# Kernel optimization log

Hardware: AMD Instinct MI355X
Metric: run time of the kernel (lower is better)

## Reference

```python
import jax, jax.numpy as jnp
from jax import lax
import numpy as np

V = 50000          # num_word; embedding table has V+1 rows
D = 512            # embedding_dim / d_model
H = 8              # nhead
FF = 2048          # dim_feedforward (hidden_dim)
L = 32             # num_label (incl START/STOP)
START, STOP = L - 2, L - 1
S = 2048           # sentence length
NEG = -10000.0


def setup_inputs() -> dict:
    k = jax.random.split(jax.random.key(0), 10)
    def rn(key, shape, s=0.02):
        return jax.random.normal(key, shape, jnp.float32) * s
    transitions = jax.random.normal(k[8], (L, L), jnp.float32)
    transitions = transitions.at[START, :].set(NEG).at[:, STOP].set(NEG)
    return {
        "sentence": jax.random.randint(k[0], (S,), 0, V + 1),
        "embed": rn(k[1], (V + 1, D), 1.0),
        "Wqkv": rn(k[2], (3 * D, D)), "bqkv": jnp.zeros((3 * D,), jnp.float32),
        "Wo": rn(k[3], (D, D)), "bo": jnp.zeros((D,), jnp.float32),
        "ln1_g": jnp.ones((D,), jnp.float32), "ln1_b": jnp.zeros((D,), jnp.float32),
        "W1": rn(k[4], (FF, D)), "b1": jnp.zeros((FF,), jnp.float32),
        "W2": rn(k[5], (D, FF)), "b2": jnp.zeros((D,), jnp.float32),
        "ln2_g": jnp.ones((D,), jnp.float32), "ln2_b": jnp.zeros((D,), jnp.float32),
        "Wt": rn(k[6], (L, D)), "bt": jnp.zeros((L,), jnp.float32),
        "transitions": transitions,
    }


def _ln(x, g, b):
    m = jnp.mean(x, -1, keepdims=True)
    v = jnp.var(x, -1, keepdims=True)
    return (x - m) * lax.rsqrt(v + 1e-5) * g + b


def _transformer_feats(sentence, embed, Wqkv, bqkv, Wo, bo, ln1_g, ln1_b,
                       W1, b1, W2, b2, ln2_g, ln2_b, Wt, bt):
    x = embed[sentence]                                   # [S, D]
    qkv = x @ Wqkv.T + bqkv                               # [S, 3D]
    q, k, v = jnp.split(qkv, 3, axis=-1)
    to_heads = lambda t: t.reshape(S, H, D // H).transpose(1, 0, 2)  # [H, S, dh]
    q, k, v = to_heads(q), to_heads(k), to_heads(v)
    att = jax.nn.softmax(jnp.einsum('hsd,htd->hst', q, k) / np.float32(np.sqrt(D // H)), axis=-1)
    o = jnp.einsum('hst,htd->hsd', att, v).transpose(1, 0, 2).reshape(S, D)
    # post-norm TransformerEncoderLayer (eval mode: dropout off), relu FFN
    x = _ln(x + o @ Wo.T + bo, ln1_g, ln1_b)
    ff = jax.nn.relu(x @ W1.T + b1) @ W2.T + b2
    x = _ln(x + ff, ln2_g, ln2_b)
    return x @ Wt.T + bt                                  # [S, L] emission scores


def _viterbi(feats, transitions):
    init = jnp.full((L,), NEG, jnp.float32).at[START].set(0.0)
    def step(prev, emit):
        scores = prev[None, :] + transitions              # [next_tag, prev_tag]
        bp = jnp.argmax(scores, axis=1)                   # best prev tag per next tag
        return jnp.max(scores, axis=1) + emit, bp
    last, bps = lax.scan(step, init, feats)               # bps: [S, L]
    terminal = last + transitions[STOP]
    best = jnp.argmax(terminal)
    def back(tag, bp):
        return bp[tag], tag
    _, path = lax.scan(back, best, bps, reverse=True)     # path[t] = best tag at step t
    return terminal[best], path


def reference(sentence, embed, Wqkv, bqkv, Wo, bo, ln1_g, ln1_b,
              W1, b1, W2, b2, ln2_g, ln2_b, Wt, bt, transitions):
    feats = _transformer_feats(sentence, embed, Wqkv, bqkv, Wo, bo, ln1_g, ln1_b,
                               W1, b1, W2, b2, ln2_g, ln2_b, Wt, bt)
    score, path = _viterbi(feats, transitions)
    return score, path
```

## Files before the change

### kernel.cpp

```cpp
#include <hip/hip_runtime.h>
#include <cstddef>

#define S_LEN 2048
#define D_MODEL 512
#define NHEAD 8
#define DH 64
#define FF_DIM 2048
#define L_TAGS 32
#define START_TAG 30
#define STOP_TAG 31
#define NEGV (-10000.0f)
#define QSCALE 0.18033688f

typedef unsigned int uint2v __attribute__((ext_vector_type(2)));
typedef __attribute__((ext_vector_type(8))) short short8v;
typedef __attribute__((ext_vector_type(4))) float f32x4;

union U8 { uint4 u; short8v s; };

__device__ __forceinline__ unsigned short f2bf(float f) {
  unsigned u = __float_as_uint(f);
  u += 0x7fff + ((u >> 16) & 1);
  return (unsigned short)(u >> 16);
}
__device__ __forceinline__ unsigned cvtpk(float lo, float hi) {
  unsigned r;
  asm("v_cvt_pk_bf16_f32 %0, %1, %2" : "=v"(r) : "v"(lo), "v"(hi));
  return r;
}

__global__ __launch_bounds__(256) void k_f2h4(const float* __restrict__ s0, short* __restrict__ d0,
                                              const float* __restrict__ s1, short* __restrict__ d1,
                                              const float* __restrict__ s2, short* __restrict__ d2,
                                              const float* __restrict__ s3, short* __restrict__ d3) {
  const int b = blockIdx.x;
  const float* src; short* dst; int i;
  if (b < 384)       { src = s0; dst = d0; i = b * 256 + threadIdx.x; }
  else if (b < 512)  { src = s1; dst = d1; i = (b - 384) * 256 + threadIdx.x; }
  else if (b < 1024) { src = s2; dst = d2; i = (b - 512) * 256 + threadIdx.x; }
  else               { src = s3; dst = d3; i = (b - 1024) * 256 + threadIdx.x; }
  f32x4 a = *(const f32x4*)(src + (size_t)i * 8);
  f32x4 c = *(const f32x4*)(src + (size_t)i * 8 + 4);
  U8 t;
  t.u.x = cvtpk(a[0], a[1]); t.u.y = cvtpk(a[2], a[3]);
  t.u.z = cvtpk(c[0], c[1]); t.u.w = cvtpk(c[2], c[3]);
  *(short8v*)(dst + (size_t)i * 8) = t.s;
}

__global__ __launch_bounds__(256, 2) void k_gemm_qkv(const int* __restrict__ sent,
                                                     const float* __restrict__ embed,
                                                     const short* __restrict__ B,
                                                     const float* __restrict__ bias,
                                                     short* __restrict__ C,
                                                     int N, int K) {
  __shared__ __align__(16) short As[2][128 * 64];
  __shared__ __align__(16) short Bs[2][128 * 64];
  const int tid = threadIdx.x;
  const int nwg = gridDim.x * gridDim.y;
  int lin = blockIdx.x + gridDim.x * blockIdx.y;
  int wk = (lin & 7) * (nwg >> 3) + (lin >> 3);
  const int bxs = wk % gridDim.x, bys = wk / gridDim.x;
  const int bm = bys * 128, bn = bxs * 128;
  const int w = tid >> 6, lane = tid & 63;
  const int wr = w >> 1, wc = w & 1;
  const int fr = lane & 15, kg = lane >> 4;
  const int srow = tid >> 1, sc0 = (tid & 1) * 4;
  const int swz = srow & 7;
  const float* gA = embed + (size_t)sent[bm + srow] * K + sc0 * 8;
  const short* gB = B + (size_t)(bn + srow) * K + sc0 * 8;
  f32x4 ra[8];
  short8v rb[4];
  f32x4 acc[4][4] = {};

  auto loadg = [&](int k0) {
#pragma unroll
    for (int c = 0; c < 4; ++c) {
      ra[2 * c] = *(const f32x4*)(gA + k0 + c * 8);
      ra[2 * c + 1] = *(const f32x4*)(gA + k0 + c * 8 + 4);
      rb[c] = *(const short8v*)(gB + k0 + c * 8);
    }
  };
  auto storeb = [&](int b) {
    short* dA = &As[b][srow * 64];
    short* dB = &Bs[b][srow * 64];
#pragma unroll
    for (int c = 0; c < 4; ++c) {
      U8 ta;
      ta.u.x = cvtpk(ra[2 * c][0], ra[2 * c][1]);
      ta.u.y = cvtpk(ra[2 * c][2], ra[2 * c][3]);
      ta.u.z = cvtpk(ra[2 * c + 1][0], ra[2 * c + 1][1]);
      ta.u.w = cvtpk(ra[2 * c + 1][2], ra[2 * c + 1][3]);
      *(short8v*)(dA + (((sc0 + c) ^ swz) << 3)) = ta.s;
      *(short8v*)(dB + (((sc0 + c) ^ swz) << 3)) = rb[c];
    }
  };

  loadg(0);
  storeb(0);
  __syncthreads();
  int cur = 0;
  const int fswz = fr & 7;
  for (int k0 = 0; k0 < K; k0 += 64) {
    const bool more = (k0 + 64) < K;
    if (more) loadg(k0 + 64);
    const short* rA = &As[cur][(wr * 64 + fr) * 64];
    const short* rB = &Bs[cur][(wc * 64 + fr) * 64];
#pragma unroll
    for (int ks = 0; ks < 2; ++ks) {
      const int co = ((ks * 4 + kg) ^ fswz) << 3;
      short8v af[4], bf[4];
#pragma unroll
      for (int rt = 0; rt < 4; ++rt) af[rt] = *(const short8v*)(rA + rt * 16 * 64 + co);
#pragma unroll
      for (int ct = 0; ct < 4; ++ct) bf[ct] = *(const short8v*)(rB + ct * 16 * 64 + co);
#pragma unroll
      for (int rt = 0; rt < 4; ++rt)
#pragma unroll
        for (int ct = 0; ct < 4; ++ct)
          acc[rt][ct] = __builtin_amdgcn_mfma_f32_16x16x32_bf16(af[rt], bf[ct], acc[rt][ct], 0, 0, 0);
    }
    if (more) storeb(cur ^ 1);
    __syncthreads();
    cur ^= 1;
  }
#pragma unroll
  for (int rt = 0; rt < 4; ++rt) {
#pragma unroll
    for (int ct = 0; ct < 4; ++ct) {
      f32x4 v = acc[rt][ct];
      const int row0 = bm + wr * 64 + rt * 16 + kg * 4;
      const int col = bn + wc * 64 + ct * 16 + fr;
      const float bs = bias[col];
#pragma unroll
      for (int j = 0; j < 4; ++j)
        C[(size_t)(row0 + j) * N + col] = (short)f2bf(v[j] + bs);
    }
  }
}

template <int RT, bool RELU, bool OBF>
__global__ __launch_bounds__(256, 2) void k_gemm_bf(const short* __restrict__ A,
                                                    const short* __restrict__ B,
                                                    const float* __restrict__ bias,
                                                    void* __restrict__ Cp,
                                                    int M, int N, int K) {
  constexpr int BM = RT * 32;
  constexpr int CH = (BM * 8) / 256;
  __shared__ __align__(16) short As[2][BM * 64];
  __shared__ __align__(16) short Bs[2][BM * 64];
  const int tid = threadIdx.x;
  const int nwg = gridDim.x * gridDim.y;
  int lin = blockIdx.x + gridDim.x * blockIdx.y;
  int wk = (lin & 7) * (nwg >> 3) + (lin >> 3);
  const int bxs = wk % gridDim.x, bys = wk / gridDim.x;
  const int bm = bys * BM, bn = bxs * BM;
  const int w = tid >> 6, lane = tid & 63;
  const int wr = w >> 1, wc = w & 1;
  const int fr = lane & 15, kg = lane >> 4;
  const int srow = (RT == 4) ? (tid >> 1) : (tid >> 2);
  const int sc0 = (RT == 4) ? ((tid & 1) * 4) : ((tid & 3) * 2);
  const int swz = srow & 7;
  const short* gA = A + (size_t)(bm + srow) * K + sc0 * 8;
  const short* gB = B + (size_t)(bn + srow) * K + sc0 * 8;
  short8v ra[CH], rb[CH];
  f32x4 acc[RT][RT] = {};

  auto loadg = [&](int k0) {
#pragma unroll
    for (int c = 0; c < CH; ++c) {
      ra[c] = *(const short8v*)(gA + k0 + c * 8);
      rb[c] = *(const short8v*)(gB + k0 + c * 8);
    }
  };
  auto storeb = [&](int b) {
    short* dA = &As[b][srow * 64];
    short* dB = &Bs[b][srow * 64];
#pragma unroll
    for (int c = 0; c < CH; ++c) {
      *(short8v*)(dA + (((sc0 + c) ^ swz) << 3)) = ra[c];
      *(short8v*)(dB + (((sc0 + c) ^ swz) << 3)) = rb[c];
    }
  };

  loadg(0);
  storeb(0);
  __syncthreads();
  int cur = 0;
  const int fswz = fr & 7;
  for (int k0 = 0; k0 < K; k0 += 64) {
    const bool more = (k0 + 64) < K;
    if (more) loadg(k0 + 64);
    const short* rA = &As[cur][(wr * (RT * 16) + fr) * 64];
    const short* rB = &Bs[cur][(wc * (RT * 16) + fr) * 64];
#pragma unroll
    for (int ks = 0; ks < 2; ++ks) {
      const int co = ((ks * 4 + kg) ^ fswz) << 3;
      short8v af[RT], bf[RT];
#pragma unroll
      for (int rt = 0; rt < RT; ++rt) af[rt] = *(const short8v*)(rA + rt * 16 * 64 + co);
#pragma unroll
      for (int ct = 0; ct < RT; ++ct) bf[ct] = *(const short8v*)(rB + ct * 16 * 64 + co);
#pragma unroll
      for (int rt = 0; rt < RT; ++rt)
#pragma unroll
        for (int ct = 0; ct < RT; ++ct)
          acc[rt][ct] = __builtin_amdgcn_mfma_f32_16x16x32_bf16(af[rt], bf[ct], acc[rt][ct], 0, 0, 0);
    }
    if (more) storeb(cur ^ 1);
    __syncthreads();
    cur ^= 1;
  }
#pragma unroll
  for (int rt = 0; rt < RT; ++rt) {
#pragma unroll
    for (int ct = 0; ct < RT; ++ct) {
      f32x4 v = acc[rt][ct];
      const int row0 = bm + wr * (RT * 16) + rt * 16 + kg * 4;
      const int col = bn + wc * (RT * 16) + ct * 16 + fr;
      const float bs = bias[col];
#pragma unroll
      for (int j = 0; j < 4; ++j) {
        float o = v[j] + bs;
        if (RELU) o = fmaxf(o, 0.f);
        if (OBF)
          ((short*)Cp)[(size_t)(row0 + j) * N + col] = (short)f2bf(o);
        else
          ((float*)Cp)[(size_t)(row0 + j) * N + col] = o;
      }
    }
  }
}

__global__ __launch_bounds__(256) void k_attn(const short* __restrict__ qkv,
                                              short* __restrict__ ob) {
  __shared__ __align__(16) short Ks[2][64 * 64];
  __shared__ __align__(16) short Vt[2][64 * 72];
  __shared__ __align__(16) short Pl[4][16 * 72];
  const int tid = threadIdx.x;
  const int b = blockIdx.x;
  const int h = b & 7;
  const int bq = (b >> 3) * 64;
  const int wq = tid >> 6, lane = tid & 63;
  const int fr = lane & 15, kg = lane >> 4;
  auto scale8 = [](short8v q) -> short8v {
    unsigned wv[4];
#pragma unroll
    for (int i = 0; i < 4; ++i) {
      float lo = __uint_as_float(((unsigned)(unsigned short)q[2 * i]) << 16) * QSCALE;
      float hi = __uint_as_float(((unsigned)(unsigned short)q[2 * i + 1]) << 16) * QSCALE;
      wv[i] = cvtpk(lo, hi);
    }
    U8 t;
    t.u.x = wv[0]; t.u.y = wv[1]; t.u.z = wv[2]; t.u.w = wv[3];
    return t.s;
  };
  short8v qf[2];
  {
    const short* qsrc = qkv + (size_t)(bq + wq * 16 + fr) * 1536 + h * DH;
    qf[0] = scale8(*(const short8v*)(qsrc + kg * 8));
    qf[1] = scale8(*(const short8v*)(qsrc + 32 + kg * 8));
  }
  float m[4], ls[4];
  f32x4 oac[4] = {};
#pragma unroll
  for (int j = 0; j < 4; ++j) { m[j] = -1e30f; ls[j] = 0.f; }

  const int srow = tid >> 2, sc0 = (tid & 3) * 2;
  const int kpair = tid & 31, dgrp = tid >> 5;
  short8v kr0, kr1, va, vb;
  auto loadt = [&](int kt) {
    const short* kbase = qkv + (size_t)(kt * 64 + srow) * 1536 + 512 + h * DH;
    kr0 = *(const short8v*)(kbase + sc0 * 8);
    kr1 = *(const short8v*)(kbase + sc0 * 8 + 8);
    const short* vbase = qkv + (size_t)(kt * 64 + 2 * kpair) * 1536 + 1024 + h * DH + dgrp * 8;
    va = *(const short8v*)(vbase);
    vb = *(const short8v*)(vbase + 1536);
  };
  auto storet = [&](int cu) {
    short* dk = &Ks[cu][srow * 64];
    *(short8v*)(dk + ((sc0 ^ (srow & 7)) << 3)) = kr0;
    *(short8v*)(dk + (((sc0 + 1) ^ (srow & 7)) << 3)) = kr1;
#pragma unroll
    for (int i = 0; i < 8; ++i) {
      unsigned u = ((unsigned)(unsigned short)va[i]) |
                   (((unsigned)(unsigned short)vb[i]) << 16);
      *(unsigned*)&Vt[cu][(dgrp * 8 + i) * 72 + 2 * kpair] = u;
    }
  };

  loadt(0);
  int cur = 0;
  for (int kt = 0; kt < 32; ++kt) {
    storet(cur);
    __syncthreads();
    if (kt < 31) loadt(kt + 1);
    f32x4 sac[4] = {};
#pragma unroll
    for (int ks = 0; ks < 2; ++ks) {
#pragma unroll
      for (int ct = 0; ct < 4; ++ct) {
        const int row = ct * 16 + fr;
        short8v bfr = *(const short8v*)&Ks[cur][row * 64 + (((ks * 4 + kg) ^ (row & 7)) << 3)];
        sac[ct] = __builtin_amdgcn_mfma_f32_16x16x32_bf16(qf[ks], bfr, sac[ct], 0, 0, 0);
      }
    }
    float pv[4][4];
#pragma unroll
    for (int j = 0; j < 4; ++j) {
      float v = fmaxf(fmaxf(sac[0][j], sac[1][j]), fmaxf(sac[2][j], sac[3][j]));
#pragma unroll
      for (int off = 1; off < 16; off <<= 1) v = fmaxf(v, __shfl_xor(v, off, 64));
      float mn = fmaxf(m[j], v);
      float f = __builtin_amdgcn_exp2f(m[j] - mn);
      m[j] = mn;
      float rs = 0.f;
#pragma unroll
      for (int ct = 0; ct < 4; ++ct) {
        pv[ct][j] = __builtin_amdgcn_exp2f(sac[ct][j] - mn);
        rs += pv[ct][j];
      }
      ls[j] = ls[j] * f + rs;
#pragma unroll
      for (int ct = 0; ct < 4; ++ct) oac[ct][j] *= f;
    }
#pragma unroll
    for (int ct = 0; ct < 4; ++ct)
#pragma unroll
      for (int j = 0; j < 4; ++j)
        Pl[wq][(kg * 4 + j) * 72 + ct * 16 + fr] = (short)f2bf(pv[ct][j]);
#pragma unroll
    for (int ks = 0; ks < 2; ++ks) {
      short8v paf = *(const short8v*)&Pl[wq][fr * 72 + ks * 32 + kg * 8];
#pragma unroll
      for (int ct = 0; ct < 4; ++ct) {
        short8v vf = *(const short8v*)&Vt[cur][(ct * 16 + fr) * 72 + ks * 32 + kg * 8];
        oac[ct] = __builtin_amdgcn_mfma_f32_16x16x32_bf16(paf, vf, oac[ct], 0, 0, 0);
      }
    }
    cur ^= 1;
  }
#pragma unroll
  for (int j = 0; j < 4; ++j) {
#pragma unroll
    for (int off = 1; off < 16; off <<= 1) ls[j] += __shfl_xor(ls[j], off, 64);
    float inv = 1.f / ls[j];
    const int q = bq + wq * 16 + kg * 4 + j;
#pragma unroll
    for (int ct = 0; ct < 4; ++ct)
      ob[(size_t)q * D_MODEL + h * DH + ct * 16 + fr] = (short)f2bf(oac[ct][j] * inv);
  }
}

__global__ __launch_bounds__(128) void k_ln(const float* __restrict__ a,
                                            const int* __restrict__ sent,
                                            const float* __restrict__ embed,
                                            const float* __restrict__ r,
                                            const float* __restrict__ g,
                                            const float* __restrict__ b,
                                            float* __restrict__ out,
                                            short* __restrict__ outh) {
  __shared__ float red[2];
  const int row = blockIdx.x, tid = threadIdx.x;
  const size_t off = (size_t)row * D_MODEL + tid * 4;
  float4 av;
  if (sent)
    av = *(const float4*)(embed + (size_t)sent[row] * D_MODEL + tid * 4);
  else
    av = *(const float4*)(a + off);
  float4 rv = *(const float4*)(r + off);
  float v0 = av.x + rv.x, v1 = av.y + rv.y, v2 = av.z + rv.z, v3 = av.w + rv.w;
  float s = v0 + v1 + v2 + v3;
#pragma unroll
  for (int d = 1; d < 64; d <<= 1) s += __shfl_xor(s, d, 64);
  if ((tid & 63) == 0) red[tid >> 6] = s;
  __syncthreads();
  float mean = (red[0] + red[1]) * (1.f / 512.f);
  __syncthreads();
  float d0 = v0 - mean, d1 = v1 - mean, d2 = v2 - mean, d3 = v3 - mean;
  float sq = d0 * d0 + d1 * d1 + d2 * d2 + d3 * d3;
#pragma unroll
  for (int d = 1; d < 64; d <<= 1) sq += __shfl_xor(sq, d, 64);
  if ((tid & 63) == 0) red[tid >> 6] = sq;
  __syncthreads();
  float inv = rsqrtf((red[0] + red[1]) * (1.f / 512.f) + 1e-5f);
  float4 gv = *(const float4*)(g + tid * 4);
  float4 bv = *(const float4*)(b + tid * 4);
  float4 o;
  o.x = d0 * inv * gv.x + bv.x;
  o.y = d1 * inv * gv.y + bv.y;
  o.z = d2 * inv * gv.z + bv.z;
  o.w = d3 * inv * gv.w + bv.w;
  *(float4*)(out + off) = o;
  if (outh) {
    uint2v t;
    t[0] = cvtpk(o.x, o.y);
    t[1] = cvtpk(o.z, o.w);
    *(uint2v*)(outh + off) = t;
  }
}

__global__ __launch_bounds__(128) void k_lnfeats(const float* __restrict__ a,
                                                 const float* __restrict__ r,
                                                 const float* __restrict__ g,
                                                 const float* __restrict__ b,
                                                 const float* __restrict__ Wt,
                                                 const float* __restrict__ bt,
                                                 float* __restrict__ feats) {
  __shared__ float red[2];
  __shared__ float part[2][32];
  const int row = blockIdx.x, tid = threadIdx.x;
  const size_t off = (size_t)row * D_MODEL + tid * 4;
  float4 av = *(const float4*)(a + off);
  float4 rv = *(const float4*)(r + off);
  float v0 = av.x + rv.x, v1 = av.y + rv.y, v2 = av.z + rv.z, v3 = av.w + rv.w;
  float s = v0 + v1 + v2 + v3;
#pragma unroll
  for (int d = 1; d < 64; d <<= 1) s += __shfl_xor(s, d, 64);
  if ((tid & 63) == 0) red[tid >> 6] = s;
  __syncthreads();
  float mean = (red[0] + red[1]) * (1.f / 512.f);
  __syncthreads();
  float d0 = v0 - mean, d1 = v1 - mean, d2 = v2 - mean, d3 = v3 - mean;
  float sq = d0 * d0 + d1 * d1 + d2 * d2 + d3 * d3;
#pragma unroll
  for (int d = 1; d < 64; d <<= 1) sq += __shfl_xor(sq, d, 64);
  if ((tid & 63) == 0) red[tid >> 6] = sq;
  __syncthreads();
  float inv = rsqrtf((red[0] + red[1]) * (1.f / 512.f) + 1e-5f);
  float4 gv = *(const float4*)(g + tid * 4);
  float4 bv = *(const float4*)(b + tid * 4);
  float4 o;
  o.x = d0 * inv * gv.x + bv.x;
  o.y = d1 * inv * gv.y + bv.y;
  o.z = d2 * inv * gv.z + bv.z;
  o.w = d3 * inv * gv.w + bv.w;
  const int lane = tid & 63, wv = tid >> 6;
#pragma unroll
  for (int l = 0; l < 32; ++l) {
    float4 wr4 = *(const float4*)(Wt + (size_t)l * D_MODEL + tid * 4);
    float p = o.x * wr4.x + o.y * wr4.y + o.z * wr4.z + o.w * wr4.w;
#pragma unroll
    for (int d = 1; d < 64; d <<= 1) p += __shfl_xor(p, d, 64);
    if (lane == 0) part[wv][l] = p;
  }
  __syncthreads();
  if (tid < 32) feats[(size_t)row * L_TAGS + tid] = part[0][tid] + part[1][tid] + bt[tid];
}

__global__ __launch_bounds__(64) void k_scan1(const float* __restrict__ feats,
                                              const float* __restrict__ T,
                                              float* __restrict__ P) {
  __shared__ float S[2][32];
  const int c = blockIdx.x >> 4;
  const int l = threadIdx.x;
  const int n = l & 31, pl = l >> 5;
  const int p = (blockIdx.x & 15) * 2 + pl;
  float Trow[32];
#pragma unroll
  for (int q = 0; q < 32; ++q) Trow[q] = T[n * 32 + q];
  const int tbase = c * 32;
  float er[4];
#pragma unroll
  for (int i = 0; i < 4; ++i) er[i] = feats[(tbase + i) * 32 + n];
  float a = T[n * 32 + p] + er[0];
  S[pl][n] = a;
  const float* fp = feats + (size_t)(tbase + 4) * 32 + n;
  er[0] = fp[0]; fp += 32;
  for (int u = 1; u < 32; ++u) {
    float e = er[u & 3];
    float enew = fp[0]; fp += 32;
    const float4* Sv = (const float4*)&S[pl][0];
    float g[32];
#pragma unroll
    for (int j4 = 0; j4 < 8; ++j4) {
      float4 sv = Sv[j4];
      g[j4 * 4 + 0] = sv.x + Trow[j4 * 4 + 0];
      g[j4 * 4 + 1] = sv.y + Trow[j4 * 4 + 1];
      g[j4 * 4 + 2] = sv.z + Trow[j4 * 4 + 2];
      g[j4 * 4 + 3] = sv.w + Trow[j4 * 4 + 3];
    }
#pragma unroll
    for (int st = 1; st < 32; st <<= 1)
#pragma unroll
      for (int j = 0; j < 32; j += 2 * st) g[j] = fmaxf(g[j], g[j + st]);
    a = g[0] + e;
    S[pl][n] = a;
    er[u & 3] = enew;
  }
  P[(size_t)c * 1024 + n * 32 + p] = a;
}

__global__ __launch_bounds__(64) void k_scan2(const float* __restrict__ P,
                                              const float* __restrict__ T,
                                              float* __restrict__ alphas,
                                              float* __restrict__ out,
                                              int* __restrict__ bestp) {
  __shared__ float Sa[32];
  const int l = threadIdx.x, n = l & 31, half = l >> 5;
  float a = (n == START_TAG) ? 0.f : NEGV;
  const float* pbase = P + n * 32 + half * 16;
  float4 pr[4];
#pragma unroll
  for (int j = 0; j < 4; ++j) pr[j] = *(const float4*)(pbase + j * 4);
  for (int c = 0; c < 64; ++c) {
    float4 nx[4];
#pragma unroll
    for (int j = 0; j < 4; ++j)
      nx[j] = *(const float4*)(pbase + (size_t)(c + 1) * 1024 + j * 4);
    alphas[(size_t)(c * 32) * 32 + n] = a;
    Sa[n] = a;
    const float4* Sv = (const float4*)&Sa[half * 16];
    float g[16];
#pragma unroll
    for (int j = 0; j < 4; ++j) {
      float4 sv = Sv[j];
      g[j * 4 + 0] = pr[j].x + sv.x;
      g[j * 4 + 1] = pr[j].y + sv.y;
      g[j * 4 + 2] = pr[j].z + sv.z;
      g[j * 4 + 3] = pr[j].w + sv.w;
    }
#pragma unroll
    for (int st = 1; st < 16; st <<= 1)
#pragma unroll
      for (int j = 0; j < 16; j += 2 * st) g[j] = fmaxf(g[j], g[j + st]);
    uint2v r = __builtin_amdgcn_permlane32_swap(__float_as_uint(g[0]),
                                                __float_as_uint(g[0]), false, false);
    a = fmaxf(__uint_as_float(r[0]), __uint_as_float(r[1]));
#pragma unroll
    for (int j = 0; j < 4; ++j) pr[j] = nx[j];
  }
  float term = a + T[STOP_TAG * 32 + n];
  float bv = term;
  int bi = n;
#pragma unroll
  for (int d = 1; d < 32; d <<= 1) {
    float ov = __shfl_xor(bv, d, 64);
    int oi = __shfl_xor(bi, d, 64);
    if (ov > bv || (ov == bv && oi < bi)) { bv = ov; bi = oi; }
  }
  if (l == 0) { out[0] = bv; *bestp = bi; }
}

__global__ __launch_bounds__(64) void k_scan3(const float* __restrict__ feats,
                                              const float* __restrict__ T,
                                              const float* __restrict__ alphas,
                                              unsigned char* __restrict__ cand,
                                              unsigned char* __restrict__ amap) {
  __shared__ float Sa[32];
  __shared__ unsigned char bpl[32][32];
  __shared__ unsigned cnd[256];
  const int c = blockIdx.x, l = threadIdx.x, n = l & 31, half = l >> 5;
  float Tr[16];
#pragma unroll
  for (int j = 0; j < 16; ++j) Tr[j] = T[n * 32 + half * 16 + j];
  const int tbase = c * 32;
  float a = alphas[(size_t)tbase * 32 + n];
  float er[4];
#pragma unroll
  for (int i = 0; i < 4; ++i) er[i] = feats[(tbase + i) * 32 + n];
  const float* fp = feats + (size_t)(tbase + 4) * 32 + n;
  Sa[n] = a;
  for (int u = 0; u < 32; ++u) {
    float e = er[u & 3];
    float enew = fp[0]; fp += 32;
    const float4* Sv = (const float4*)&Sa[half * 16];
    float4 s0 = Sv[0], s1 = Sv[1], s2 = Sv[2], s3 = Sv[3];
    float v[16] = {s0.x + Tr[0],  s0.y + Tr[1],  s0.z + Tr[2],  s0.w + Tr[3],
                   s1.x + Tr[4],  s1.y + Tr[5],  s1.z + Tr[6],  s1.w + Tr[7],
                   s2.x + Tr[8],  s2.y + Tr[9],  s2.z + Tr[10], s2.w + Tr[11],
                   s3.x + Tr[12], s3.y + Tr[13], s3.z + Tr[14], s3.w + Tr[15]};
    int id[16];
#pragma unroll
    for (int j = 0; j < 16; ++j) id[j] = half * 16 + j;
#pragma unroll
    for (int st = 1; st < 16; st <<= 1)
#pragma unroll
      for (int j = 0; j < 16; j += 2 * st)
        if (v[j + st] > v[j]) { v[j] = v[j + st]; id[j] = id[j + st]; }
    uint2v rv = __builtin_amdgcn_permlane32_swap(__float_as_uint(v[0]),
                                                 __float_as_uint(v[0]), false, false);
    uint2v ri = __builtin_amdgcn_permlane32_swap((unsigned)id[0], (unsigned)id[0],
                                                 false, false);
    float v0 = __uint_as_float(rv[0]), v1 = __uint_as_float(rv[1]);
    int i0 = (int)ri[0], i1 = (int)ri[1];
    float wvv = (v1 > v0) ? v1 : v0;
    int wi = (v1 > v0) ? i1 : i0;
    bpl[u][n] = (unsigned char)wi;
    a = wvv + e;
    Sa[n] = a;
    er[u & 3] = enew;
  }
  unsigned char* cnb = (unsigned char*)cnd;
  int tg = n;
  cnb[n * 32 + 31] = (unsigned char)n;
  for (int j = 31; j >= 1; --j) {
    tg = bpl[j][tg];
    cnb[n * 32 + (j - 1)] = (unsigned char)tg;
  }
  if (half == 0) amap[c * 32 + n] = bpl[0][tg];
#pragma unroll
  for (int i = 0; i < 4; ++i)
    ((unsigned*)(cand + (size_t)c * 1024))[l * 4 + i] = cnd[l * 4 + i];
}

__global__ __launch_bounds__(256) void k_trace2(const unsigned char* __restrict__ amap,
                                                const unsigned char* __restrict__ cand,
                                                const int* __restrict__ bestp,
                                                float* __restrict__ outp) {
  __shared__ unsigned char Am[64][32];
  __shared__ unsigned char et[64];
  const int tid = threadIdx.x;
  ((unsigned*)&Am[0][0])[tid] = ((const unsigned*)amap)[tid];
  ((unsigned*)&Am[32][0])[tid] = ((const unsigned*)amap)[tid + 256];
  __syncthreads();
  for (int d = 1; d < 64; d <<= 1) {
    unsigned char tmpv[8];
#pragma unroll
    for (int i = 0; i < 8; ++i) {
      int id = tid + 256 * i;
      int cc = id >> 5, e = id & 31;
      tmpv[i] = (cc + d < 64) ? Am[cc][Am[cc + d][e]] : Am[cc][e];
    }
    __syncthreads();
#pragma unroll
    for (int i = 0; i < 8; ++i) {
      int id = tid + 256 * i;
      Am[id >> 5][id & 31] = tmpv[i];
    }
    __syncthreads();
  }
  const int best = *bestp;
  if (tid < 64) et[tid] = (tid == 63) ? (unsigned char)best : Am[tid + 1][best];
  __syncthreads();
#pragma unroll
  for (int i = 0; i < 8; ++i) {
    int t = tid + 256 * i;
    int cc = t >> 5, j = t & 31;
    outp[1 + t] = (float)cand[(size_t)cc * 1024 + (size_t)et[cc] * 32 + j];
  }
}

extern "C" void kernel_launch(void* const* d_in, const int* in_sizes, int n_in,
                              void* d_out, int out_size, void* d_ws, size_t ws_size,
                              hipStream_t stream) {
  (void)in_sizes; (void)n_in; (void)out_size; (void)ws_size;
  const int* sent = (const int*)d_in[0];
  const float* embed = (const float*)d_in[1];
  const float* Wqkv = (const float*)d_in[2];
  const float* bqkv = (const float*)d_in[3];
  const float* Wo = (const float*)d_in[4];
  const float* bo = (const float*)d_in[5];
  const float* g1 = (const float*)d_in[6];
  const float* b1n = (const float*)d_in[7];
  const float* W1 = (const float*)d_in[8];
  const float* b1f = (const float*)d_in[9];
  const float* W2 = (const float*)d_in[10];
  const float* b2f = (const float*)d_in[11];
  const float* g2 = (const float*)d_in[12];
  const float* b2n = (const float*)d_in[13];
  const float* Wt = (const float*)d_in[14];
  const float* bt = (const float*)d_in[15];
  const float* T = (const float*)d_in[16];
  float* out = (float*)d_out;

  float* ws = (float*)d_ws;
  const size_t M1 = 1u << 20;
  short* qkvh = (short*)ws;
  short* obh = (short*)(ws + 2 * M1);
  float* yb = ws + 3 * M1;
  float* x1 = ws + 4 * M1;
  short* x1h = (short*)(ws + 5 * M1);
  short* ffbh = (short*)(ws + 6 * M1);
  float* zb = ws + 8 * M1;
  short* wqkvh = (short*)(ws + 10 * M1);
  short* woh = wqkvh + 786432;
  short* w1h = woh + 262144;
  short* w2h = w1h + 1048576;
  float* feats = ws + 11 * M1;
  float* alphas = feats + 2048 * 32 + 64;
  float* P = alphas + 2049 * 32 + 64;
  int* bestp = (int*)(P + 65 * 1024 + 64);
  unsigned char* cand = (unsigned char*)(bestp + 64);
  unsigned char* amap = cand + 2048 * 32;

  k_f2h4<<<dim3(1536), dim3(256), 0, stream>>>(Wqkv, wqkvh, Wo, woh, W1, w1h, W2, w2h);
  k_gemm_qkv<<<dim3(12, 16), dim3(256), 0, stream>>>(sent, embed, wqkvh, bqkv, qkvh, 1536, 512);
  k_attn<<<dim3(256), dim3(256), 0, stream>>>(qkvh, obh);
  k_gemm_bf<2, false, false><<<dim3(8, 32), dim3(256), 0, stream>>>(obh, woh, bo, yb, 2048, 512, 512);
  k_ln<<<dim3(2048), dim3(128), 0, stream>>>(nullptr, sent, embed, yb, g1, b1n, x1, x1h);
  k_gemm_bf<4, true, true><<<dim3(16, 16), dim3(256), 0, stream>>>(x1h, w1h, b1f, ffbh, 2048, 2048, 512);
  k_gemm_bf<2, false, false><<<dim3(8, 32), dim3(256), 0, stream>>>(ffbh, w2h, b2f, zb, 2048, 512, 2048);
  k_lnfeats<<<dim3(2048), dim3(128), 0, stream>>>(x1, zb, g2, b2n, Wt, bt, feats);
  k_scan1<<<dim3(1024), dim3(64), 0, stream>>>(feats, T, P);
  k_scan2<<<dim3(1), dim3(64), 0, stream>>>(P, T, alphas, out, bestp);
  k_scan3<<<dim3(64), dim3(64), 0, stream>>>(feats, T, alphas, cand, amap);
  k_trace2<<<dim3(1), dim3(256), 0, stream>>>(amap, cand, bestp, out);
}
```

Before: 179.1 us.

## Halve attention query tile to 32 rows, add MFMA priority and lazy rescale

The attention kernel now runs 512 blocks of 128 threads, each covering 32 query rows instead of 64, so more blocks are available to fill the compute units. Each thread now loads four K chunks and two V pairs per tile. MFMA sections are wrapped in s_setprio so matrix work is favoured over other waves. The online softmax skips the rescale of the output accumulator when no row maximum increases across the wavefront. The cost is that every K/V tile is loaded twice as often overall, raising global and LDS traffic per unit of compute.

Result: slower. 206.4 us (+15.2%).

```diff
diff --git a/kernel.cpp b/kernel.cpp
--- a/kernel.cpp
+++ b/kernel.cpp
@@ -231,15 +231,15 @@
   }
 }
 
-__global__ __launch_bounds__(256) void k_attn(const short* __restrict__ qkv,
+__global__ __launch_bounds__(128) void k_attn(const short* __restrict__ qkv,
                                               short* __restrict__ ob) {
   __shared__ __align__(16) short Ks[2][64 * 64];
   __shared__ __align__(16) short Vt[2][64 * 72];
-  __shared__ __align__(16) short Pl[4][16 * 72];
+  __shared__ __align__(16) short Pl[2][16 * 72];
   const int tid = threadIdx.x;
   const int b = blockIdx.x;
   const int h = b & 7;
-  const int bq = (b >> 3) * 64;
+  const int bq = (b >> 3) * 32;
   const int wq = tid >> 6, lane = tid & 63;
   const int fr = lane & 15, kg = lane >> 4;
   auto scale8 = [](short8v q) -> short8v {
@@ -265,26 +265,32 @@
 #pragma unroll
   for (int j = 0; j < 4; ++j) { m[j] = -1e30f; ls[j] = 0.f; }
 
-  const int srow = tid >> 2, sc0 = (tid & 3) * 2;
+  const int srow = tid >> 1, sc0 = (tid & 1) * 4;
   const int kpair = tid & 31, dgrp = tid >> 5;
-  short8v kr0, kr1, va, vb;
+  short8v kr[4], va0, vb0, va1, vb1;
   auto loadt = [&](int kt) {
     const short* kbase = qkv + (size_t)(kt * 64 + srow) * 1536 + 512 + h * DH;
-    kr0 = *(const short8v*)(kbase + sc0 * 8);
-    kr1 = *(const short8v*)(kbase + sc0 * 8 + 8);
+#pragma unroll
+    for (int c = 0; c < 4; ++c) kr[c] = *(const short8v*)(kbase + (sc0 + c) * 8);
     const short* vbase = qkv + (size_t)(kt * 64 + 2 * kpair) * 1536 + 1024 + h * DH + dgrp * 8;
-    va = *(const short8v*)(vbase);
-    vb = *(const short8v*)(vbase + 1536);
+    va0 = *(const short8v*)(vbase);
+    vb0 = *(const short8v*)(vbase + 1536);
+    va1 = *(const short8v*)(vbase + 32);
+    vb1 = *(const short8v*)(vbase + 1536 + 32);
   };
   auto storet = [&](int cu) {
     short* dk = &Ks[cu][srow * 64];
-    *(short8v*)(dk + ((sc0 ^ (srow & 7)) << 3)) = kr0;
-    *(short8v*)(dk + (((sc0 + 1) ^ (srow & 7)) << 3)) = kr1;
+#pragma unroll
+    for (int c = 0; c < 4; ++c)
+      *(short8v*)(dk + (((sc0 + c) ^ (srow & 7)) << 3)) = kr[c];
 #pragma unroll
     for (int i = 0; i < 8; ++i) {
-      unsigned u = ((unsigned)(unsigned short)va[i]) |
-                   (((unsigned)(unsigned short)vb[i]) << 16);
-      *(unsigned*)&Vt[cu][(dgrp * 8 + i) * 72 + 2 * kpair] = u;
+      unsigned u0 = ((unsigned)(unsigned short)va0[i]) |
+                    (((unsigned)(unsigned short)vb0[i]) << 16);
+      unsigned u1 = ((unsigned)(unsigned short)va1[i]) |
+                    (((unsigned)(unsigned short)vb1[i]) << 16);
+      *(unsigned*)&Vt[cu][(dgrp * 8 + i) * 72 + 2 * kpair] = u0;
+      *(unsigned*)&Vt[cu][((dgrp + 4) * 8 + i) * 72 + 2 * kpair] = u1;
     }
   };
 
@@ -295,6 +301,7 @@
     __syncthreads();
     if (kt < 31) loadt(kt + 1);
     f32x4 sac[4] = {};
+    __builtin_amdgcn_s_setprio(1);
 #pragma unroll
     for (int ks = 0; ks < 2; ++ks) {
 #pragma unroll
@@ -304,30 +311,41 @@
         sac[ct] = __builtin_amdgcn_mfma_f32_16x16x32_bf16(qf[ks], bfr, sac[ct], 0, 0, 0);
       }
     }
+    __builtin_amdgcn_s_setprio(0);
     float pv[4][4];
 #pragma unroll
     for (int j = 0; j < 4; ++j) {
       float v = fmaxf(fmaxf(sac[0][j], sac[1][j]), fmaxf(sac[2][j], sac[3][j]));
 #pragma unroll
       for (int off = 1; off < 16; off <<= 1) v = fmaxf(v, __shfl_xor(v, off, 64));
-      float mn = fmaxf(m[j], v);
-      float f = __builtin_amdgcn_exp2f(m[j] - mn);
-      m[j] = mn;
       float rs = 0.f;
-#pragma unroll
-      for (int ct = 0; ct < 4; ++ct) {
-        pv[ct][j] = __builtin_amdgcn_exp2f(sac[ct][j] - mn);
-        rs += pv[ct][j];
+      if (__all(v <= m[j])) {
+#pragma unroll
+        for (int ct = 0; ct < 4; ++ct) {
+          pv[ct][j] = __builtin_amdgcn_exp2f(sac[ct][j] - m[j]);
+          rs += pv[ct][j];
+        }
+        ls[j] += rs;
+      } else {
+        float mn = fmaxf(m[j], v);
+        float f = __builtin_amdgcn_exp2f(m[j] - mn);
+        m[j] = mn;
+#pragma unroll
+        for (int ct = 0; ct < 4; ++ct) {
+          pv[ct][j] = __builtin_amdgcn_exp2f(sac[ct][j] - mn);
+          rs += pv[ct][j];
+        }
+        ls[j] = ls[j] * f + rs;
+#pragma unroll
+        for (int ct = 0; ct < 4; ++ct) oac[ct][j] *= f;
       }
-      ls[j] = ls[j] * f + rs;
-#pragma unroll
-      for (int ct = 0; ct < 4; ++ct) oac[ct][j] *= f;
     }
 #pragma unroll
     for (int ct = 0; ct < 4; ++ct)
 #pragma unroll
       for (int j = 0; j < 4; ++j)
         Pl[wq][(kg * 4 + j) * 72 + ct * 16 + fr] = (short)f2bf(pv[ct][j]);
+    __builtin_amdgcn_s_setprio(1);
 #pragma unroll
     for (int ks = 0; ks < 2; ++ks) {
       short8v paf = *(const short8v*)&Pl[wq][fr * 72 + ks * 32 + kg * 8];
@@ -337,6 +355,7 @@
         oac[ct] = __builtin_amdgcn_mfma_f32_16x16x32_bf16(paf, vf, oac[ct], 0, 0, 0);
       }
     }
+    __builtin_amdgcn_s_setprio(0);
     cur ^= 1;
   }
 #pragma unroll
@@ -685,7 +704,7 @@
 
   k_f2h4<<<dim3(1536), dim3(256), 0, stream>>>(Wqkv, wqkvh, Wo, woh, W1, w1h, W2, w2h);
   k_gemm_qkv<<<dim3(12, 16), dim3(256), 0, stream>>>(sent, embed, wqkvh, bqkv, qkvh, 1536, 512);
-  k_attn<<<dim3(256), dim3(256), 0, stream>>>(qkvh, obh);
+  k_attn<<<dim3(512), dim3(128), 0, stream>>>(qkvh, obh);
   k_gemm_bf<2, false, false><<<dim3(8, 32), dim3(256), 0, stream>>>(obh, woh, bo, yb, 2048, 512, 512);
   k_ln<<<dim3(2048), dim3(128), 0, stream>>>(nullptr, sent, embed, yb, g1, b1n, x1, x1h);
   k_gemm_bf<4, true, true><<<dim3(16, 16), dim3(256), 0, stream>>>(x1h, w1h, b1f, ffbh, 2048, 2048, 512);
```
